# Kernel optimization log

Hardware: AMD Instinct MI355X
Metric: run time of the kernel (lower is better)

The kernel has to match this reference:

```python
import jax, jax.numpy as jnp
import numpy as np

N = 50000
E = 800000
F_IN = 512
HID = 32
HEADS = 8
CLS = 64
NEG_SLOPE = 0.2
EPS = 1e-16  # PyG softmax denominator epsilon


def setup_inputs() -> dict:
    key = jax.random.key(0)
    ks = jax.random.split(key, 10)
    x = jax.random.normal(ks[0], (N, F_IN), dtype=jnp.float32)
    edge_index = jax.random.randint(ks[1], (2, E), 0, N, dtype=jnp.int64)
    # layer 1: in=F_IN, heads=HEADS, out_per_head=HID, concat
    s1 = 1.0 / np.sqrt(F_IN)
    W1 = jax.random.normal(ks[2], (F_IN, HEADS * HID), dtype=jnp.float32) * s1
    att_src1 = jax.random.normal(ks[3], (HEADS, HID), dtype=jnp.float32) * 0.1
    att_dst1 = jax.random.normal(ks[4], (HEADS, HID), dtype=jnp.float32) * 0.1
    b1 = jnp.zeros((HEADS * HID,), dtype=jnp.float32)
    # layer 2: in=HEADS*HID, heads=1, out=CLS, no concat
    s2 = 1.0 / np.sqrt(HEADS * HID)
    W2 = jax.random.normal(ks[5], (HEADS * HID, CLS), dtype=jnp.float32) * s2
    att_src2 = jax.random.normal(ks[6], (1, CLS), dtype=jnp.float32) * 0.1
    att_dst2 = jax.random.normal(ks[7], (1, CLS), dtype=jnp.float32) * 0.1
    b2 = jnp.zeros((CLS,), dtype=jnp.float32)
    return {"x": x, "edge_index": edge_index,
            "W1": W1, "att_src1": att_src1, "att_dst1": att_dst1, "b1": b1,
            "W2": W2, "att_src2": att_src2, "att_dst2": att_dst2, "b2": b2}


def gat_conv(x, edge_index, W, att_src, att_dst, bias, concat):
    n = x.shape[0]
    heads, c = att_src.shape
    h = (x @ W).reshape(n, heads, c)                       # [N,H,C]
    # add self loops (PyG GATConv default)
    loop = jnp.arange(n, dtype=edge_index.dtype)
    src = jnp.concatenate([edge_index[0], loop])
    dst = jnp.concatenate([edge_index[1], loop])
    a_src = jnp.einsum('nhc,hc->nh', h, att_src)           # [N,H]
    a_dst = jnp.einsum('nhc,hc->nh', h, att_dst)
    e = a_src[src] + a_dst[dst]                            # [E',H]
    e = jax.nn.leaky_relu(e, NEG_SLOPE)
    # segment softmax over destination node
    m = jax.ops.segment_max(e, dst, num_segments=n)
    e = jnp.exp(e - jax.lax.stop_gradient(m)[dst])
    s = jax.ops.segment_sum(e, dst, num_segments=n)
    alpha = e / (s[dst] + EPS)                             # [E',H]
    msg = h[src] * alpha[:, :, None]                       # [E',H,C]
    out = jax.ops.segment_sum(msg, dst, num_segments=n)    # [N,H,C]
    out = out.reshape(n, heads * c) if concat else out.mean(axis=1)
    return out + bias


def reference(x, edge_index, W1, att_src1, att_dst1, b1, W2, att_src2, att_dst2, b2):
    h = gat_conv(x, edge_index, W1, att_src1, att_dst1, b1, concat=True)
    h = jax.nn.relu(h)
    # F.dropout with training=False (eval) is identity
    h = gat_conv(h, edge_index, W2, att_src2, att_dst2, b2, concat=False)
    return jax.nn.log_softmax(h, axis=1)
```

## Files before the change

kernel.cpp:

```cpp
#include <hip/hip_runtime.h>
#include <hip/hip_bf16.h>
#include <stdint.h>

#define F_IN 512
#define HID 32
#define HEADS 8
#define C1 (HEADS*HID)
#define CLS 64
#define NEG 0.2f
#define EPS 1e-16f

typedef __bf16 bf16x8 __attribute__((ext_vector_type(8)));
typedef __bf16 bf16x4 __attribute__((ext_vector_type(4)));
typedef float  f32x4  __attribute__((ext_vector_type(4)));

__device__ __forceinline__ float leaky(float v) { return v > 0.f ? v : NEG * v; }

__device__ __forceinline__ bf16x8 cvt8(float4 a, float4 b) {
  bf16x8 o;
  o[0] = (__bf16)a.x; o[1] = (__bf16)a.y; o[2] = (__bf16)a.z; o[3] = (__bf16)a.w;
  o[4] = (__bf16)b.x; o[5] = (__bf16)b.y; o[6] = (__bf16)b.z; o[7] = (__bf16)b.w;
  return o;
}

__global__ __launch_bounds__(256) void prep(const float* __restrict__ W1,
    const float* __restrict__ W2, const int* __restrict__ ei,
    __bf16* __restrict__ w1t, __bf16* __restrict__ w2t,
    int* __restrict__ deg, int E) {
  const int b = blockIdx.x, t = threadIdx.x;
  if (b < 64) {
    int i = b * 256 + t;
    int o0 = i * 8;
    int c = o0 >> 9, k0 = o0 & 511;
    bf16x8 o;
#pragma unroll
    for (int j = 0; j < 8; j++) o[j] = (__bf16)W1[(size_t)(k0 + j) * C1 + c];
    *(bf16x8*)(w1t + (size_t)o0) = o;
  } else if (b < 72) {
    int i = (b - 64) * 256 + t;
    int o0 = i * 8;
    int c = o0 >> 8, k0 = o0 & 255;
    bf16x8 o;
#pragma unroll
    for (int j = 0; j < 8; j++) o[j] = (__bf16)W2[(size_t)(k0 + j) * CLS + c];
    *(bf16x8*)(w2t + (size_t)o0) = o;
  } else {
    int e = (b - 72) * 256 + t;
    if (e < E) atomicAdd(&deg[ei[E + e]], 1);
  }
}

__global__ __launch_bounds__(256) void scan_k1(const int* __restrict__ deg,
    int* __restrict__ bsum, int N) {
  __shared__ int ws[4];
  const int t = threadIdx.x, lane = t & 63, wid = t >> 6;
  int i = blockIdx.x * 256 + t;
  int v = (i < N) ? deg[i] : 0;
#pragma unroll
  for (int o = 1; o < 64; o <<= 1) v += __shfl_xor(v, o);
  if (lane == 0) ws[wid] = v;
  __syncthreads();
  if (t == 0) bsum[blockIdx.x] = ws[0] + ws[1] + ws[2] + ws[3];
}

__global__ __launch_bounds__(256) void scan_k2(int* __restrict__ bsum, int nb) {
  __shared__ int wsum[4];
  __shared__ int carry_s;
  const int t = threadIdx.x, lane = t & 63, wid = t >> 6;
  if (t == 0) carry_s = 0;
  __syncthreads();
  for (int base = 0; base < nb; base += 256) {
    int i = base + t;
    int v = (i < nb) ? bsum[i] : 0;
    int inc = v;
#pragma unroll
    for (int o = 1; o < 64; o <<= 1) { int x = __shfl_up(inc, o); if (lane >= o) inc += x; }
    if (lane == 63) wsum[wid] = inc;
    __syncthreads();
    int woff = 0;
    for (int w = 0; w < wid; w++) woff += wsum[w];
    int excl = carry_s + woff + inc - v;
    if (i < nb) bsum[i] = excl;
    __syncthreads();
    if (t == 0) carry_s += wsum[0] + wsum[1] + wsum[2] + wsum[3];
    __syncthreads();
  }
}

__global__ __launch_bounds__(256) void scan_k3(const int* __restrict__ deg,
    const int* __restrict__ bsum, int* __restrict__ rowstart,
    int* __restrict__ cur, int N) {
  __shared__ int wsum[4];
  const int t = threadIdx.x, lane = t & 63, wid = t >> 6;
  int i = blockIdx.x * 256 + t;
  int v = (i < N) ? deg[i] : 0;
  int inc = v;
#pragma unroll
  for (int o = 1; o < 64; o <<= 1) { int x = __shfl_up(inc, o); if (lane >= o) inc += x; }
  if (lane == 63) wsum[wid] = inc;
  __syncthreads();
  int woff = 0;
  for (int w = 0; w < wid; w++) woff += wsum[w];
  int excl = bsum[blockIdx.x] + woff + inc - v;
  if (i < N) { rowstart[i] = excl; cur[i] = excl; }
  if (i == N - 1) rowstart[N] = excl + v;
}

__global__ __launch_bounds__(256) void scatter_csr(const int* __restrict__ ei,
    int* __restrict__ cur, int* __restrict__ csr_src, int E) {
  int e = blockIdx.x * 256 + threadIdx.x;
  if (e >= E) return;
  int s = ei[e], d = ei[E + e];
  int pos = atomicAdd(&cur[d], 1);
  csr_src[pos] = s;
}

__global__ __launch_bounds__(256) void gemm1_mfma(const float* __restrict__ A,
    const __bf16* __restrict__ Bt, __bf16* __restrict__ C, int M) {
  __shared__ __bf16 Al[128 * 32];
  __shared__ __bf16 Bl[128 * 32];
  const int tid  = threadIdx.x;
  const int lane = tid & 63;
  const int wave = tid >> 6;
  const int lm = lane & 15, q = lane >> 4;
  const int wr = (wave >> 1) * 64, wc = (wave & 1) * 64;
  const int bm = blockIdx.y * 128, bn = blockIdx.x * 128;

  const int srow = tid >> 2;
  const int skc  = (tid & 3) * 8;

  f32x4 acc[4][4];
#pragma unroll
  for (int i = 0; i < 4; i++)
#pragma unroll
    for (int j = 0; j < 4; j++) acc[i][j] = (f32x4){0.f, 0.f, 0.f, 0.f};

  const int ra0 = min(bm + srow, M - 1);
  const int ra1 = min(bm + srow + 64, M - 1);
  const int rb0 = bn + srow, rb1 = bn + srow + 64;

  float4 a0x, a0y, a1x, a1y;
  bf16x8 vb0, vb1;
  a0x = *(const float4*)(A + (size_t)ra0 * 512 + skc);
  a0y = *(const float4*)(A + (size_t)ra0 * 512 + skc + 4);
  a1x = *(const float4*)(A + (size_t)ra1 * 512 + skc);
  a1y = *(const float4*)(A + (size_t)ra1 * 512 + skc + 4);
  vb0 = *(const bf16x8*)(Bt + (size_t)rb0 * 512 + skc);
  vb1 = *(const bf16x8*)(Bt + (size_t)rb1 * 512 + skc);

  for (int kk = 0; kk < 16; kk++) {
    __syncthreads();
    *(bf16x8*)(Al + srow * 32 + skc)        = cvt8(a0x, a0y);
    *(bf16x8*)(Al + (srow + 64) * 32 + skc) = cvt8(a1x, a1y);
    *(bf16x8*)(Bl + srow * 32 + skc)        = vb0;
    *(bf16x8*)(Bl + (srow + 64) * 32 + skc) = vb1;
    __syncthreads();
    if (kk + 1 < 16) {
      const int k0 = (kk + 1) * 32;
      a0x = *(const float4*)(A + (size_t)ra0 * 512 + k0 + skc);
      a0y = *(const float4*)(A + (size_t)ra0 * 512 + k0 + skc + 4);
      a1x = *(const float4*)(A + (size_t)ra1 * 512 + k0 + skc);
      a1y = *(const float4*)(A + (size_t)ra1 * 512 + k0 + skc + 4);
      vb0 = *(const bf16x8*)(Bt + (size_t)rb0 * 512 + k0 + skc);
      vb1 = *(const bf16x8*)(Bt + (size_t)rb1 * 512 + k0 + skc);
    }
    bf16x8 af[4], bfr[4];
#pragma unroll
    for (int mi = 0; mi < 4; mi++)
      af[mi] = *(const bf16x8*)(Al + (wr + mi * 16 + lm) * 32 + q * 8);
#pragma unroll
    for (int ni = 0; ni < 4; ni++)
      bfr[ni] = *(const bf16x8*)(Bl + (wc + ni * 16 + lm) * 32 + q * 8);
#pragma unroll
    for (int mi = 0; mi < 4; mi++)
#pragma unroll
      for (int ni = 0; ni < 4; ni++)
        acc[mi][ni] = __builtin_amdgcn_mfma_f32_16x16x32_bf16(af[mi], bfr[ni], acc[mi][ni], 0, 0, 0);
  }

#pragma unroll
  for (int mi = 0; mi < 4; mi++) {
#pragma unroll
    for (int ni = 0; ni < 4; ni++) {
      const int col = bn + wc + ni * 16 + lm;
#pragma unroll
      for (int r = 0; r < 4; r++) {
        const int row = bm + wr + mi * 16 + q * 4 + r;
        if (row < M) C[(size_t)row * C1 + col] = (__bf16)acc[mi][ni][r];
      }
    }
  }
}

__global__ __launch_bounds__(256) void gemm2_mfma(const __bf16* __restrict__ A,
    const __bf16* __restrict__ Bt, __bf16* __restrict__ C, int M) {
  __shared__ __bf16 Al[128 * 32];
  __shared__ __bf16 Bl[64 * 32];
  const int tid  = threadIdx.x;
  const int lane = tid & 63;
  const int wave = tid >> 6;
  const int lm = lane & 15, q = lane >> 4;
  const int wr = (wave >> 1) * 64, wc = (wave & 1) * 32;
  const int bm = blockIdx.x * 128;

  const int srow = tid >> 2;
  const int skc  = (tid & 3) * 8;

  f32x4 acc[4][2];
#pragma unroll
  for (int i = 0; i < 4; i++)
#pragma unroll
    for (int j = 0; j < 2; j++) acc[i][j] = (f32x4){0.f, 0.f, 0.f, 0.f};

  const int ra0 = min(bm + srow, M - 1);
  const int ra1 = min(bm + srow + 64, M - 1);

  bf16x8 va0, va1, vb;
  va0 = *(const bf16x8*)(A + (size_t)ra0 * C1 + skc);
  va1 = *(const bf16x8*)(A + (size_t)ra1 * C1 + skc);
  vb  = *(const bf16x8*)(Bt + (size_t)srow * C1 + skc);

  for (int kk = 0; kk < 8; kk++) {
    __syncthreads();
    *(bf16x8*)(Al + srow * 32 + skc)        = va0;
    *(bf16x8*)(Al + (srow + 64) * 32 + skc) = va1;
    *(bf16x8*)(Bl + srow * 32 + skc)        = vb;
    __syncthreads();
    if (kk + 1 < 8) {
      const int k0 = (kk + 1) * 32;
      va0 = *(const bf16x8*)(A + (size_t)ra0 * C1 + k0 + skc);
      va1 = *(const bf16x8*)(A + (size_t)ra1 * C1 + k0 + skc);
      vb  = *(const bf16x8*)(Bt + (size_t)srow * C1 + k0 + skc);
    }
    bf16x8 af[4], bfr[2];
#pragma unroll
    for (int mi = 0; mi < 4; mi++)
      af[mi] = *(const bf16x8*)(Al + (wr + mi * 16 + lm) * 32 + q * 8);
#pragma unroll
    for (int ni = 0; ni < 2; ni++)
      bfr[ni] = *(const bf16x8*)(Bl + (wc + ni * 16 + lm) * 32 + q * 8);
#pragma unroll
    for (int mi = 0; mi < 4; mi++)
#pragma unroll
      for (int ni = 0; ni < 2; ni++)
        acc[mi][ni] = __builtin_amdgcn_mfma_f32_16x16x32_bf16(af[mi], bfr[ni], acc[mi][ni], 0, 0, 0);
  }

#pragma unroll
  for (int mi = 0; mi < 4; mi++) {
#pragma unroll
    for (int ni = 0; ni < 2; ni++) {
      const int col = wc + ni * 16 + lm;
#pragma unroll
      for (int r = 0; r < 4; r++) {
        const int row = bm + wr + mi * 16 + q * 4 + r;
        if (row < M) C[(size_t)row * CLS + col] = (__bf16)acc[mi][ni][r];
      }
    }
  }
}

__global__ __launch_bounds__(256) void att_scores1(const __bf16* __restrict__ h1,
    const float* __restrict__ asw, const float* __restrict__ adw,
    float* __restrict__ a_src, float* __restrict__ a_dst, int N) {
  const int t = threadIdx.x, lane = t & 63;
  const int n = blockIdx.x * 4 + (t >> 6);
  if (n >= N) return;
  bf16x4 x = *(const bf16x4*)(h1 + (size_t)n * C1 + lane * 4);
  const float4 wsv = *(const float4*)(asw + lane * 4);
  const float4 wdv = *(const float4*)(adw + lane * 4);
  float ps = (float)x[0] * wsv.x + (float)x[1] * wsv.y + (float)x[2] * wsv.z + (float)x[3] * wsv.w;
  float pd = (float)x[0] * wdv.x + (float)x[1] * wdv.y + (float)x[2] * wdv.z + (float)x[3] * wdv.w;
#pragma unroll
  for (int o = 1; o <= 4; o <<= 1) { ps += __shfl_xor(ps, o); pd += __shfl_xor(pd, o); }
  if ((lane & 7) == 0) {
    a_src[(size_t)n * 8 + (lane >> 3)] = ps;
    a_dst[(size_t)n * 8 + (lane >> 3)] = pd;
  }
}

__global__ __launch_bounds__(256) void att_scores2(const __bf16* __restrict__ h2b,
    const float* __restrict__ asw, const float* __restrict__ adw,
    float* __restrict__ a_src, float* __restrict__ a_dst, int N) {
  const int t = threadIdx.x, lane = t & 63;
  const int n = blockIdx.x * 4 + (t >> 6);
  if (n >= N) return;
  float v  = (float)h2b[(size_t)n * CLS + lane];
  float ps = v * asw[lane];
  float pd = v * adw[lane];
#pragma unroll
  for (int o = 1; o < 64; o <<= 1) { ps += __shfl_xor(ps, o); pd += __shfl_xor(pd, o); }
  if (lane == 0) { a_src[n] = ps; a_dst[n] = pd; }
}

__global__ __launch_bounds__(256) void gather1(const int* __restrict__ rowstart,
    const int* __restrict__ csr_src, const __bf16* __restrict__ h1,
    const float* __restrict__ as1, const float* __restrict__ ad1,
    const float* __restrict__ b1, __bf16* __restrict__ o1, int N) {
  const int t = threadIdx.x;
  const int d = blockIdx.x * 4 + (t >> 6);
  if (d >= N) return;
  const int lane = t & 63;
  const int e8 = lane >> 3, hh = lane & 7;
  const int r0 = rowstart[d];
  const int deg = rowstart[d + 1] - r0;

  const float addh = ad1[(size_t)d * 8 + hh];
  const float self_sc = leaky(as1[(size_t)d * 8 + hh] + addh);

  int   se[8];
  float sc[8];
#pragma unroll
  for (int ch = 0; ch < 8; ch++) {
    const int j = ch * 8 + e8;
    se[ch] = 0; sc[ch] = -3.4e38f;
    if (j < deg) {
      int s = csr_src[r0 + j];
      se[ch] = s;
      sc[ch] = leaky(as1[(size_t)s * 8 + hh] + addh);
    }
  }
  float mx = -3.4e38f;
#pragma unroll
  for (int ch = 0; ch < 8; ch++) mx = fmaxf(mx, sc[ch]);
  for (int j0 = 64; j0 < deg; j0 += 8) {
    int j = j0 + e8;
    if (j < deg) {
      int s = csr_src[r0 + j];
      mx = fmaxf(mx, leaky(as1[(size_t)s * 8 + hh] + addh));
    }
  }
  mx = fmaxf(mx, __shfl_xor(mx, 8));
  mx = fmaxf(mx, __shfl_xor(mx, 16));
  mx = fmaxf(mx, __shfl_xor(mx, 32));
  mx = fmaxf(mx, self_sc);

  float sum = 0.f;
#pragma unroll
  for (int ch = 0; ch < 8; ch++)
    if (ch * 8 + e8 < deg) sum += __expf(sc[ch] - mx);
  for (int j0 = 64; j0 < deg; j0 += 8) {
    int j = j0 + e8;
    if (j < deg) {
      int s = csr_src[r0 + j];
      sum += __expf(leaky(as1[(size_t)s * 8 + hh] + addh) - mx);
    }
  }
  sum += __shfl_xor(sum, 8);
  sum += __shfl_xor(sum, 16);
  sum += __shfl_xor(sum, 32);
  sum += __expf(self_sc - mx);
  const float inv = 1.f / (sum + EPS);

  float al[8];
#pragma unroll
  for (int ch = 0; ch < 8; ch++) al[ch] = __expf(sc[ch] - mx) * inv;
  const float al_self_byhh = __expf(self_sc - mx) * inv;

  const int p = lane >> 5, g = lane & 31, hg = g >> 2;
  float acc[8];
#pragma unroll
  for (int i = 0; i < 8; i++) acc[i] = 0.f;

#pragma unroll
  for (int it = 0; it < 32; it++) {
    if (it * 2 < deg) {
      const int   j   = it * 2 + p;
      const int   s_j = __shfl(se[it >> 2], (j & 7) * 8);
      const float a_j = __shfl(al[it >> 2], (j & 7) * 8 + hg);
      bf16x8 x = *(const bf16x8*)(h1 + (size_t)s_j * C1 + g * 8);
#pragma unroll
      for (int i = 0; i < 8; i++) acc[i] += a_j * (float)x[i];
    }
  }
  for (int j0 = 64; j0 < deg; j0 += 8) {
    int j = j0 + e8;
    int se2 = 0; float al2 = 0.f;
    if (j < deg) { se2 = csr_src[r0 + j]; al2 = __expf(leaky(as1[(size_t)se2 * 8 + hh] + addh) - mx) * inv; }
#pragma unroll
    for (int it = 0; it < 4; it++) {
      if (j0 + it * 2 < deg) {
        const int   jj  = it * 2 + p;
        const int   s_j = __shfl(se2, jj * 8);
        const float a_j = __shfl(al2, jj * 8 + hg);
        bf16x8 x = *(const bf16x8*)(h1 + (size_t)s_j * C1 + g * 8);
#pragma unroll
        for (int i = 0; i < 8; i++) acc[i] += a_j * (float)x[i];
      }
    }
  }
#pragma unroll
  for (int i = 0; i < 8; i++) acc[i] += __shfl_xor(acc[i], 32);

  const float a_selfh = __shfl(al_self_byhh, hg);
  if (lane < 32) {
    bf16x8 xs = *(const bf16x8*)(h1 + (size_t)d * C1 + g * 8);
    const float4 b4a = *(const float4*)(b1 + g * 8);
    const float4 b4b = *(const float4*)(b1 + g * 8 + 4);
    bf16x8 o;
    o[0] = (__bf16)fmaxf(acc[0] + a_selfh * (float)xs[0] + b4a.x, 0.f);
    o[1] = (__bf16)fmaxf(acc[1] + a_selfh * (float)xs[1] + b4a.y, 0.f);
    o[2] = (__bf16)fmaxf(acc[2] + a_selfh * (float)xs[2] + b4a.z, 0.f);
    o[3] = (__bf16)fmaxf(acc[3] + a_selfh * (float)xs[3] + b4a.w, 0.f);
    o[4] = (__bf16)fmaxf(acc[4] + a_selfh * (float)xs[4] + b4b.x, 0.f);
    o[5] = (__bf16)fmaxf(acc[5] + a_selfh * (float)xs[5] + b4b.y, 0.f);
    o[6] = (__bf16)fmaxf(acc[6] + a_selfh * (float)xs[6] + b4b.z, 0.f);
    o[7] = (__bf16)fmaxf(acc[7] + a_selfh * (float)xs[7] + b4b.w, 0.f);
    *(bf16x8*)(o1 + (size_t)d * C1 + g * 8) = o;
  }
}

__global__ __launch_bounds__(256) void gather2(const int* __restrict__ rowstart,
    const int* __restrict__ csr_src, const __bf16* __restrict__ h2b,
    const float* __restrict__ as2, const float* __restrict__ ad2,
    const float* __restrict__ b2, float* __restrict__ out, int N) {
  const int t = threadIdx.x, lane = t & 63;
  const int d = blockIdx.x * 4 + (t >> 6);
  if (d >= N) return;
  const int r0 = rowstart[d], deg = rowstart[d + 1] - r0;
  const float addd = ad2[d];
  const float self_sc = leaky(as2[d] + addd);

  int se = 0; float sc = -3.4e38f;
  if (lane < deg) { se = csr_src[r0 + lane]; sc = leaky(as2[se] + addd); }
  float mx = sc;
  for (int j0 = 64; j0 < deg; j0 += 64) {
    int j = j0 + lane;
    if (j < deg) mx = fmaxf(mx, leaky(as2[csr_src[r0 + j]] + addd));
  }
#pragma unroll
  for (int o = 1; o < 64; o <<= 1) mx = fmaxf(mx, __shfl_xor(mx, o));
  mx = fmaxf(mx, self_sc);

  float ex = (lane < deg) ? __expf(sc - mx) : 0.f;
  float sum = ex;
  for (int j0 = 64; j0 < deg; j0 += 64) {
    int j = j0 + lane;
    if (j < deg) sum += __expf(leaky(as2[csr_src[r0 + j]] + addd) - mx);
  }
#pragma unroll
  for (int o = 1; o < 64; o <<= 1) sum += __shfl_xor(sum, o);
  const float e_self = __expf(self_sc - mx);
  sum += e_self;
  const float inv = 1.f / (sum + EPS);
  const float alpha = ex * inv;
  const float al_self = e_self * inv;

  const int e8 = lane >> 3, c8 = lane & 7;
  float acc[8];
#pragma unroll
  for (int i = 0; i < 8; i++) acc[i] = 0.f;

#pragma unroll
  for (int it = 0; it < 8; it++) {
    if (it * 8 < deg) {
      const int   j   = it * 8 + e8;
      const int   s_j = __shfl(se, j);
      const float a_j = __shfl(alpha, j);
      bf16x8 x = *(const bf16x8*)(h2b + (size_t)s_j * CLS + c8 * 8);
#pragma unroll
      for (int i = 0; i < 8; i++) acc[i] += a_j * (float)x[i];
    }
  }
  for (int j0 = 64; j0 < deg; j0 += 64) {
    int j = j0 + lane;
    int se2 = 0; float al2 = 0.f;
    if (j < deg) { se2 = csr_src[r0 + j]; al2 = __expf(leaky(as2[se2] + addd) - mx) * inv; }
#pragma unroll
    for (int it = 0; it < 8; it++) {
      if (j0 + it * 8 < deg) {
        const int   jj  = it * 8 + e8;
        const int   s_j = __shfl(se2, jj);
        const float a_j = __shfl(al2, jj);
        bf16x8 x = *(const bf16x8*)(h2b + (size_t)s_j * CLS + c8 * 8);
#pragma unroll
        for (int i = 0; i < 8; i++) acc[i] += a_j * (float)x[i];
      }
    }
  }
#pragma unroll
  for (int i = 0; i < 8; i++) {
    acc[i] += __shfl_xor(acc[i], 8);
    acc[i] += __shfl_xor(acc[i], 16);
    acc[i] += __shfl_xor(acc[i], 32);
  }

  bf16x8 xs = *(const bf16x8*)(h2b + (size_t)d * CLS + c8 * 8);
  const float4 bba = *(const float4*)(b2 + c8 * 8);
  const float4 bbb = *(const float4*)(b2 + c8 * 8 + 4);
  float v[8];
  v[0] = acc[0] + al_self * (float)xs[0] + bba.x;
  v[1] = acc[1] + al_self * (float)xs[1] + bba.y;
  v[2] = acc[2] + al_self * (float)xs[2] + bba.z;
  v[3] = acc[3] + al_self * (float)xs[3] + bba.w;
  v[4] = acc[4] + al_self * (float)xs[4] + bbb.x;
  v[5] = acc[5] + al_self * (float)xs[5] + bbb.y;
  v[6] = acc[6] + al_self * (float)xs[6] + bbb.z;
  v[7] = acc[7] + al_self * (float)xs[7] + bbb.w;
  float m2 = v[0];
#pragma unroll
  for (int i = 1; i < 8; i++) m2 = fmaxf(m2, v[i]);
  m2 = fmaxf(m2, __shfl_xor(m2, 1));
  m2 = fmaxf(m2, __shfl_xor(m2, 2));
  m2 = fmaxf(m2, __shfl_xor(m2, 4));
  float sm = 0.f;
#pragma unroll
  for (int i = 0; i < 8; i++) sm += __expf(v[i] - m2);
  sm += __shfl_xor(sm, 1);
  sm += __shfl_xor(sm, 2);
  sm += __shfl_xor(sm, 4);
  const float lg = m2 + __logf(sm);
  if (lane < 8) {
    float4 o0, o1v;
    o0.x  = v[0] - lg; o0.y  = v[1] - lg; o0.z  = v[2] - lg; o0.w  = v[3] - lg;
    o1v.x = v[4] - lg; o1v.y = v[5] - lg; o1v.z = v[6] - lg; o1v.w = v[7] - lg;
    *(float4*)(out + (size_t)d * CLS + c8 * 8)     = o0;
    *(float4*)(out + (size_t)d * CLS + c8 * 8 + 4) = o1v;
  }
}

extern "C" void kernel_launch(void* const* d_in, const int* in_sizes, int n_in,
                              void* d_out, int out_size, void* d_ws, size_t ws_size,
                              hipStream_t stream) {
  const float* x        = (const float*)d_in[0];
  const int*   ei       = (const int*)d_in[1];
  const float* W1       = (const float*)d_in[2];
  const float* att_src1 = (const float*)d_in[3];
  const float* att_dst1 = (const float*)d_in[4];
  const float* b1       = (const float*)d_in[5];
  const float* W2       = (const float*)d_in[6];
  const float* att_src2 = (const float*)d_in[7];
  const float* att_dst2 = (const float*)d_in[8];
  const float* b2       = (const float*)d_in[9];
  float* out = (float*)d_out;

  const int N  = in_sizes[0] / F_IN;
  const int E  = in_sizes[1] / 2;
  const int NB = (N + 255) / 256;

  char* ws = (char*)d_ws;
  size_t off = 0;
  auto alloc = [&](size_t bytes) -> void* {
    void* p = ws + off;
    off += (bytes + 255) & ~(size_t)255;
    return p;
  };
  __bf16* h1  = (__bf16*)alloc((size_t)N * C1 * 2);
  __bf16* o1  = (__bf16*)alloc((size_t)N * C1 * 2);
  float*  as1 = (float*)alloc((size_t)N * HEADS * 4);
  float*  ad1 = (float*)alloc((size_t)N * HEADS * 4);
  __bf16* h2b = (__bf16*)alloc((size_t)N * CLS * 2);
  float*  as2 = (float*)alloc((size_t)N * 4);
  float*  ad2 = (float*)alloc((size_t)N * 4);
  int* deg      = (int*)alloc((size_t)N * 4);
  int* rowstart = (int*)alloc((size_t)(N + 1) * 4);
  int* cur      = (int*)alloc((size_t)N * 4);
  int* csr_src  = (int*)alloc((size_t)E * 4);
  int* bsum     = (int*)alloc((size_t)NB * 4);
  __bf16* w1t = (__bf16*)alloc((size_t)C1 * F_IN * 2);
  __bf16* w2t = (__bf16*)alloc((size_t)CLS * C1 * 2);

  hipMemsetAsync(deg, 0, (size_t)N * 4, stream);
  prep<<<72 + (E + 255) / 256, 256, 0, stream>>>(W1, W2, ei, w1t, w2t, deg, E);

  scan_k1<<<NB, 256, 0, stream>>>(deg, bsum, N);
  scan_k2<<<1, 256, 0, stream>>>(bsum, NB);
  scan_k3<<<NB, 256, 0, stream>>>(deg, bsum, rowstart, cur, N);
  scatter_csr<<<(E + 255) / 256, 256, 0, stream>>>(ei, cur, csr_src, E);

  {
    dim3 g(C1 / 128, (N + 127) / 128);
    gemm1_mfma<<<g, 256, 0, stream>>>(x, w1t, h1, N);
  }
  att_scores1<<<(N + 3) / 4, 256, 0, stream>>>(h1, att_src1, att_dst1, as1, ad1, N);
  gather1<<<(N + 3) / 4, 256, 0, stream>>>(rowstart, csr_src, h1, as1, ad1, b1, o1, N);

  gemm2_mfma<<<(N + 127) / 128, 256, 0, stream>>>(o1, w2t, h2b, N);
  att_scores2<<<(N + 3) / 4, 256, 0, stream>>>(h2b, att_src2, att_dst2, as2, ad2, N);
  gather2<<<(N + 3) / 4, 256, 0, stream>>>(rowstart, csr_src, h2b, as2, ad2, b2, out, N);
}
```

Measured before the change: 414.9 us.

## Fuse attention score computation into both GEMM epilogues

Both GEMM kernels now compute the per-node source and destination attention dot products in their epilogue from the fp32 accumulators, using lane shuffles and, for layer 2, a small shared-memory cross-wave reduction. This removes the two separate att_scores kernel launches and their re-reads of h1 and h2. Layer 1's GEMM now has each block cover all 256 output columns, so the fp32 input x is read once rather than twice. The cost is twice the accumulator registers per thread, which may lower occupancy, and fewer blocks in the layer-1 grid. Scores are now computed from fp32 accumulators instead of bf16-rounded outputs, so values shift slightly.

```diff
diff --git a/kernel.cpp b/kernel.cpp
--- a/kernel.cpp
+++ b/kernel.cpp
@@ -115,96 +115,140 @@
   csr_src[pos] = s;
 }
 
-__global__ __launch_bounds__(256) void gemm1_mfma(const float* __restrict__ A,
-    const __bf16* __restrict__ Bt, __bf16* __restrict__ C, int M) {
+__global__ __launch_bounds__(256) void gemm1_fused(const float* __restrict__ A,
+    const __bf16* __restrict__ Bt, __bf16* __restrict__ C,
+    const float* __restrict__ asw, const float* __restrict__ adw,
+    float* __restrict__ a_src, float* __restrict__ a_dst, int M) {
   __shared__ __bf16 Al[128 * 32];
-  __shared__ __bf16 Bl[128 * 32];
-  const int tid  = threadIdx.x;
-  const int lane = tid & 63;
-  const int wave = tid >> 6;
+  __shared__ __bf16 Bl[256 * 32];
+  const int tid = threadIdx.x, lane = tid & 63, wave = tid >> 6;
   const int lm = lane & 15, q = lane >> 4;
-  const int wr = (wave >> 1) * 64, wc = (wave & 1) * 64;
-  const int bm = blockIdx.y * 128, bn = blockIdx.x * 128;
-
-  const int srow = tid >> 2;
-  const int skc  = (tid & 3) * 8;
-
-  f32x4 acc[4][4];
-#pragma unroll
-  for (int i = 0; i < 4; i++)
-#pragma unroll
-    for (int j = 0; j < 4; j++) acc[i][j] = (f32x4){0.f, 0.f, 0.f, 0.f};
+  const int wr = (wave >> 1) * 64, wc0 = (wave & 1) * 64;
+  const int bm = blockIdx.x * 128;
+  const int srow = tid >> 2, skc = (tid & 3) * 8;
+
+  f32x4 acc[2][4][4];
+#pragma unroll
+  for (int hf = 0; hf < 2; hf++)
+#pragma unroll
+    for (int i = 0; i < 4; i++)
+#pragma unroll
+      for (int j = 0; j < 4; j++) acc[hf][i][j] = (f32x4){0.f, 0.f, 0.f, 0.f};
 
   const int ra0 = min(bm + srow, M - 1);
   const int ra1 = min(bm + srow + 64, M - 1);
-  const int rb0 = bn + srow, rb1 = bn + srow + 64;
-
-  float4 a0x, a0y, a1x, a1y;
-  bf16x8 vb0, vb1;
-  a0x = *(const float4*)(A + (size_t)ra0 * 512 + skc);
-  a0y = *(const float4*)(A + (size_t)ra0 * 512 + skc + 4);
-  a1x = *(const float4*)(A + (size_t)ra1 * 512 + skc);
-  a1y = *(const float4*)(A + (size_t)ra1 * 512 + skc + 4);
-  vb0 = *(const bf16x8*)(Bt + (size_t)rb0 * 512 + skc);
-  vb1 = *(const bf16x8*)(Bt + (size_t)rb1 * 512 + skc);
+
+  float4 a00, a01, a10, a11;
+  bf16x8 vb[4];
+  a00 = *(const float4*)(A + (size_t)ra0 * 512 + skc);
+  a01 = *(const float4*)(A + (size_t)ra0 * 512 + skc + 4);
+  a10 = *(const float4*)(A + (size_t)ra1 * 512 + skc);
+  a11 = *(const float4*)(A + (size_t)ra1 * 512 + skc + 4);
+#pragma unroll
+  for (int rr = 0; rr < 4; rr++)
+    vb[rr] = *(const bf16x8*)(Bt + (size_t)(srow + rr * 64) * 512 + skc);
 
   for (int kk = 0; kk < 16; kk++) {
     __syncthreads();
-    *(bf16x8*)(Al + srow * 32 + skc)        = cvt8(a0x, a0y);
-    *(bf16x8*)(Al + (srow + 64) * 32 + skc) = cvt8(a1x, a1y);
-    *(bf16x8*)(Bl + srow * 32 + skc)        = vb0;
-    *(bf16x8*)(Bl + (srow + 64) * 32 + skc) = vb1;
+    *(bf16x8*)(Al + srow * 32 + skc)        = cvt8(a00, a01);
+    *(bf16x8*)(Al + (srow + 64) * 32 + skc) = cvt8(a10, a11);
+#pragma unroll
+    for (int rr = 0; rr < 4; rr++)
+      *(bf16x8*)(Bl + (srow + rr * 64) * 32 + skc) = vb[rr];
     __syncthreads();
     if (kk + 1 < 16) {
       const int k0 = (kk + 1) * 32;
-      a0x = *(const float4*)(A + (size_t)ra0 * 512 + k0 + skc);
-      a0y = *(const float4*)(A + (size_t)ra0 * 512 + k0 + skc + 4);
-      a1x = *(const float4*)(A + (size_t)ra1 * 512 + k0 + skc);
-      a1y = *(const float4*)(A + (size_t)ra1 * 512 + k0 + skc + 4);
-      vb0 = *(const bf16x8*)(Bt + (size_t)rb0 * 512 + k0 + skc);
-      vb1 = *(const bf16x8*)(Bt + (size_t)rb1 * 512 + k0 + skc);
-    }
-    bf16x8 af[4], bfr[4];
+      a00 = *(const float4*)(A + (size_t)ra0 * 512 + k0 + skc);
+      a01 = *(const float4*)(A + (size_t)ra0 * 512 + k0 + skc + 4);
+      a10 = *(const float4*)(A + (size_t)ra1 * 512 + k0 + skc);
+      a11 = *(const float4*)(A + (size_t)ra1 * 512 + k0 + skc + 4);
+#pragma unroll
+      for (int rr = 0; rr < 4; rr++)
+        vb[rr] = *(const bf16x8*)(Bt + (size_t)(srow + rr * 64) * 512 + k0 + skc);
+    }
+    bf16x8 af[4];
 #pragma unroll
     for (int mi = 0; mi < 4; mi++)
       af[mi] = *(const bf16x8*)(Al + (wr + mi * 16 + lm) * 32 + q * 8);
 #pragma unroll
-    for (int ni = 0; ni < 4; ni++)
-      bfr[ni] = *(const bf16x8*)(Bl + (wc + ni * 16 + lm) * 32 + q * 8);
-#pragma unroll
-    for (int mi = 0; mi < 4; mi++)
+    for (int hf = 0; hf < 2; hf++) {
+      bf16x8 bfr[4];
 #pragma unroll
       for (int ni = 0; ni < 4; ni++)
-        acc[mi][ni] = __builtin_amdgcn_mfma_f32_16x16x32_bf16(af[mi], bfr[ni], acc[mi][ni], 0, 0, 0);
-  }
-
-#pragma unroll
-  for (int mi = 0; mi < 4; mi++) {
+        bfr[ni] = *(const bf16x8*)(Bl + (wc0 + hf * 128 + ni * 16 + lm) * 32 + q * 8);
+#pragma unroll
+      for (int mi = 0; mi < 4; mi++)
+#pragma unroll
+        for (int ni = 0; ni < 4; ni++)
+          acc[hf][mi][ni] = __builtin_amdgcn_mfma_f32_16x16x32_bf16(af[mi], bfr[ni], acc[hf][mi][ni], 0, 0, 0);
+    }
+  }
+
+#pragma unroll
+  for (int hf = 0; hf < 2; hf++) {
+#pragma unroll
+    for (int mi = 0; mi < 4; mi++) {
+#pragma unroll
+      for (int ni = 0; ni < 4; ni++) {
+        const int col = wc0 + hf * 128 + ni * 16 + lm;
+#pragma unroll
+        for (int r = 0; r < 4; r++) {
+          const int row = bm + wr + mi * 16 + q * 4 + r;
+          if (row < M) C[(size_t)row * C1 + col] = (__bf16)acc[hf][mi][ni][r];
+        }
+      }
+    }
+  }
+
+#pragma unroll
+  for (int hf = 0; hf < 2; hf++) {
+    const int cb = wc0 + hf * 128;
+    const int h0 = cb >> 5;
+    float ws[4], wd[4];
 #pragma unroll
     for (int ni = 0; ni < 4; ni++) {
-      const int col = bn + wc + ni * 16 + lm;
+      ws[ni] = asw[cb + ni * 16 + lm];
+      wd[ni] = adw[cb + ni * 16 + lm];
+    }
+#pragma unroll
+    for (int mi = 0; mi < 4; mi++) {
 #pragma unroll
       for (int r = 0; r < 4; r++) {
-        const int row = bm + wr + mi * 16 + q * 4 + r;
-        if (row < M) C[(size_t)row * C1 + col] = (__bf16)acc[mi][ni][r];
+        float ps0 = acc[hf][mi][0][r] * ws[0] + acc[hf][mi][1][r] * ws[1];
+        float ps1 = acc[hf][mi][2][r] * ws[2] + acc[hf][mi][3][r] * ws[3];
+        float pd0 = acc[hf][mi][0][r] * wd[0] + acc[hf][mi][1][r] * wd[1];
+        float pd1 = acc[hf][mi][2][r] * wd[2] + acc[hf][mi][3][r] * wd[3];
+#pragma unroll
+        for (int o = 1; o <= 8; o <<= 1) {
+          ps0 += __shfl_xor(ps0, o); ps1 += __shfl_xor(ps1, o);
+          pd0 += __shfl_xor(pd0, o); pd1 += __shfl_xor(pd1, o);
+        }
+        if (lm == 0) {
+          const int row = bm + wr + mi * 16 + q * 4 + r;
+          if (row < M) {
+            a_src[(size_t)row * 8 + h0]     = ps0;
+            a_src[(size_t)row * 8 + h0 + 1] = ps1;
+            a_dst[(size_t)row * 8 + h0]     = pd0;
+            a_dst[(size_t)row * 8 + h0 + 1] = pd1;
+          }
+        }
       }
     }
   }
 }
 
-__global__ __launch_bounds__(256) void gemm2_mfma(const __bf16* __restrict__ A,
-    const __bf16* __restrict__ Bt, __bf16* __restrict__ C, int M) {
+__global__ __launch_bounds__(256) void gemm2_fused(const __bf16* __restrict__ A,
+    const __bf16* __restrict__ Bt, __bf16* __restrict__ C,
+    const float* __restrict__ asw, const float* __restrict__ adw,
+    float* __restrict__ a_src, float* __restrict__ a_dst, int M) {
   __shared__ __bf16 Al[128 * 32];
   __shared__ __bf16 Bl[64 * 32];
-  const int tid  = threadIdx.x;
-  const int lane = tid & 63;
-  const int wave = tid >> 6;
+  __shared__ float sred[128][2][2];
+  const int tid = threadIdx.x, lane = tid & 63, wave = tid >> 6;
   const int lm = lane & 15, q = lane >> 4;
   const int wr = (wave >> 1) * 64, wc = (wave & 1) * 32;
   const int bm = blockIdx.x * 128;
-
-  const int srow = tid >> 2;
-  const int skc  = (tid & 3) * 8;
+  const int srow = tid >> 2, skc = (tid & 3) * 8;
 
   f32x4 acc[4][2];
 #pragma unroll
@@ -246,6 +290,12 @@
         acc[mi][ni] = __builtin_amdgcn_mfma_f32_16x16x32_bf16(af[mi], bfr[ni], acc[mi][ni], 0, 0, 0);
   }
 
+  float ws[2], wd[2];
+#pragma unroll
+  for (int ni = 0; ni < 2; ni++) {
+    ws[ni] = asw[wc + ni * 16 + lm];
+    wd[ni] = adw[wc + ni * 16 + lm];
+  }
 #pragma unroll
   for (int mi = 0; mi < 4; mi++) {
 #pragma unroll
@@ -257,40 +307,27 @@
         if (row < M) C[(size_t)row * CLS + col] = (__bf16)acc[mi][ni][r];
       }
     }
-  }
-}
-
-__global__ __launch_bounds__(256) void att_scores1(const __bf16* __restrict__ h1,
-    const float* __restrict__ asw, const float* __restrict__ adw,
-    float* __restrict__ a_src, float* __restrict__ a_dst, int N) {
-  const int t = threadIdx.x, lane = t & 63;
-  const int n = blockIdx.x * 4 + (t >> 6);
-  if (n >= N) return;
-  bf16x4 x = *(const bf16x4*)(h1 + (size_t)n * C1 + lane * 4);
-  const float4 wsv = *(const float4*)(asw + lane * 4);
-  const float4 wdv = *(const float4*)(adw + lane * 4);
-  float ps = (float)x[0] * wsv.x + (float)x[1] * wsv.y + (float)x[2] * wsv.z + (float)x[3] * wsv.w;
-  float pd = (float)x[0] * wdv.x + (float)x[1] * wdv.y + (float)x[2] * wdv.z + (float)x[3] * wdv.w;
-#pragma unroll
-  for (int o = 1; o <= 4; o <<= 1) { ps += __shfl_xor(ps, o); pd += __shfl_xor(pd, o); }
-  if ((lane & 7) == 0) {
-    a_src[(size_t)n * 8 + (lane >> 3)] = ps;
-    a_dst[(size_t)n * 8 + (lane >> 3)] = pd;
-  }
-}
-
-__global__ __launch_bounds__(256) void att_scores2(const __bf16* __restrict__ h2b,
-    const float* __restrict__ asw, const float* __restrict__ adw,
-    float* __restrict__ a_src, float* __restrict__ a_dst, int N) {
-  const int t = threadIdx.x, lane = t & 63;
-  const int n = blockIdx.x * 4 + (t >> 6);
-  if (n >= N) return;
-  float v  = (float)h2b[(size_t)n * CLS + lane];
-  float ps = v * asw[lane];
-  float pd = v * adw[lane];
-#pragma unroll
-  for (int o = 1; o < 64; o <<= 1) { ps += __shfl_xor(ps, o); pd += __shfl_xor(pd, o); }
-  if (lane == 0) { a_src[n] = ps; a_dst[n] = pd; }
+#pragma unroll
+    for (int r = 0; r < 4; r++) {
+      float ps = acc[mi][0][r] * ws[0] + acc[mi][1][r] * ws[1];
+      float pd = acc[mi][0][r] * wd[0] + acc[mi][1][r] * wd[1];
+#pragma unroll
+      for (int o = 1; o <= 8; o <<= 1) { ps += __shfl_xor(ps, o); pd += __shfl_xor(pd, o); }
+      if (lm == 0) {
+        const int rl = wr + mi * 16 + q * 4 + r;
+        sred[rl][wave & 1][0] = ps;
+        sred[rl][wave & 1][1] = pd;
+      }
+    }
+  }
+  __syncthreads();
+  if (tid < 128) {
+    const int row = bm + tid;
+    if (row < M) {
+      a_src[row] = sred[tid][0][0] + sred[tid][1][0];
+      a_dst[row] = sred[tid][0][1] + sred[tid][1][1];
+    }
+  }
 }
 
 __global__ __launch_bounds__(256) void gather1(const int* __restrict__ rowstart,
@@ -568,14 +605,9 @@
   scan_k3<<<NB, 256, 0, stream>>>(deg, bsum, rowstart, cur, N);
   scatter_csr<<<(E + 255) / 256, 256, 0, stream>>>(ei, cur, csr_src, E);
 
-  {
-    dim3 g(C1 / 128, (N + 127) / 128);
-    gemm1_mfma<<<g, 256, 0, stream>>>(x, w1t, h1, N);
-  }
-  att_scores1<<<(N + 3) / 4, 256, 0, stream>>>(h1, att_src1, att_dst1, as1, ad1, N);
+  gemm1_fused<<<(N + 127) / 128, 256, 0, stream>>>(x, w1t, h1, att_src1, att_dst1, as1, ad1, N);
   gather1<<<(N + 3) / 4, 256, 0, stream>>>(rowstart, csr_src, h1, as1, ad1, b1, o1, N);
 
-  gemm2_mfma<<<(N + 127) / 128, 256, 0, stream>>>(o1, w2t, h2b, N);
-  att_scores2<<<(N + 3) / 4, 256, 0, stream>>>(h2b, att_src2, att_dst2, as2, ad2, N);
+  gemm2_fused<<<(N + 127) / 128, 256, 0, stream>>>(o1, w2t, h2b, att_src2, att_dst2, as2, ad2, N);
   gather2<<<(N + 3) / 4, 256, 0, stream>>>(rowstart, csr_src, h2b, as2, ad2, b2, out, N);
 }
```

New measurement: 413.0 us. No clear change (-0.5%).
